# Performance work log

Hardware: AMD Instinct MI355X
Metric: run time of the kernel (lower is better)

Reference implementation:

```python
import jax, jax.numpy as jnp
import numpy as np


def setup_inputs() -> dict:
    key = jax.random.key(0)
    k1, k2, k3, k4 = jax.random.split(key, 4)
    B, T, IN, D = 32, 256, 64, 128
    x = jax.random.normal(k1, (B, T, IN), dtype=jnp.float32)
    h0 = jnp.zeros((B, D), dtype=jnp.float32)
    Wx = jax.random.normal(k2, (IN, D), dtype=jnp.float32) * 0.01
    Wgate = jax.random.normal(k3, (D, D), dtype=jnp.float32) * 0.01
    Wh = jax.random.normal(k4, (D, D), dtype=jnp.float32) * 0.01
    return {"x": x, "h0": h0, "Wx": Wx, "Wgate": Wgate, "Wh": Wh}


def reference(x, h0, Wx, Wgate, Wh):
    # x: (B, T, in_dim); h0: (B, dim); returns (h_final, y, hidden_grads, dh_dWh)
    def step_single(h_r, x_r):
        # per-sample gated update: h_r (dim,), x_r (in_dim,)
        pre = x_r @ Wx + h_r @ Wh
        a = jax.nn.gelu(pre, approximate=False)  # torch GELU() is the exact erf variant
        g = jax.nn.sigmoid(a @ Wgate)
        hn = g * h_r + (1.0 - g)
        return hn, hn

    # per-step, per-sample Jacobian d h_new / d h  (mirrors vmap(jacrev(..., argnums=1)))
    jac_batched = jax.vmap(jax.jacrev(step_single, argnums=0, has_aux=True))

    def body(h, x_t):  # h: (B, dim), x_t: (B, in_dim)
        jac, h_new = jac_batched(h, x_t)  # jac: (B, dim, dim)
        return h_new, (h_new, jac)

    xt = jnp.swapaxes(x, 0, 1)  # (T, B, in_dim)
    h_final, (ys, jacs) = jax.lax.scan(body, h0, xt)
    y = jnp.swapaxes(ys, 0, 1)  # (B, T, dim)

    # last-step Jacobian wrt Wh, evaluated with the post-update h (as in the torch code)
    x_last = x[:, -1, :]

    def f_wh(Wh_):
        pre = x_last @ Wx + h_final @ Wh_
        a = jax.nn.gelu(pre, approximate=False)
        g = jax.nn.sigmoid(a @ Wgate)
        return g * h_final + (1.0 - g)

    dh_dWh = jax.jacrev(f_wh)(Wh)  # (B, dim, dim, dim)
    return (h_final, y, jacs, dh_dWh)
```

## Files before the change

### kernel.cpp

```cpp
#include <hip/hip_runtime.h>


#define JACOFF 1052672L
#define DHWOFF 135270400L

typedef __attribute__((ext_vector_type(8))) short frag_ab;
typedef __attribute__((ext_vector_type(4))) float frag_cd;

__device__ __forceinline__ short f2bf(float f) {
    unsigned u = __builtin_bit_cast(unsigned, f);
    unsigned r = (u + 0x7fffu + ((u >> 16) & 1u)) >> 16;
    return (short)r;
}

__global__ __launch_bounds__(256) void prep_xw_kernel(
    const float* __restrict__ Wh, const float* __restrict__ Wg,
    const float* __restrict__ x, const float* __restrict__ Wx,
    float* __restrict__ whT, float* __restrict__ wgT, float* __restrict__ xw)
{
    int blk = blockIdx.x;
    int tid = threadIdx.x;
    if (blk < 128) {
        int idx = blk * 256 + tid;
        if (idx < 16384) {
            int k = idx >> 7, i = idx & 127;
            whT[i * 128 + k] = Wh[idx];
        } else {
            int r = idx - 16384;
            int k = r >> 7, i = r & 127;
            wgT[i * 128 + k] = Wg[r];
        }
        return;
    }
    __shared__ float xs[2][64];
    int sub = tid >> 7;
    int bt = (blk - 128) * 2 + sub;
    int i = tid & 127;
    if (i < 64) xs[sub][i] = x[bt * 64 + i];
    __syncthreads();
    float acc = 0.f;
#pragma unroll
    for (int m = 0; m < 64; ++m)
        acc += xs[sub][m] * Wx[m * 128 + i];
    xw[bt * 128 + i] = acc;
}

__global__ __launch_bounds__(512, 1) void scan_pk_kernel(
    const float* __restrict__ xw, const float* __restrict__ h0,
    const float* __restrict__ whT, const float* __restrict__ wgT,
    const float* __restrict__ Wgate, const float* __restrict__ Wh,
    float* __restrict__ out,
    short* __restrict__ Abf, float* __restrict__ wgv, float* __restrict__ wc,
    float* __restrict__ wdF, float* __restrict__ wuF, float* __restrict__ whF,
    short* __restrict__ PT)
{
    int tid = threadIdx.x;
    if (blockIdx.x >= 32) {
        int c = (blockIdx.x - 32) * 32 + (tid >> 4);
        int k0 = (tid & 15) * 8;
        int i = c >> 7, j = c & 127;
        short v[8];
#pragma unroll
        for (int m = 0; m < 8; ++m) {
            float wg = Wgate[(k0 + m) * 128 + i];
            float wh = Wh[j * 128 + k0 + m];
            v[m] = f2bf(wg * wh);
        }
        *(frag_ab*)(PT + (long)c * 128 + k0) = *(frag_ab*)v;
        return;
    }

    const int b = blockIdx.x;
    const int i = tid >> 2, qtr = tid & 3;
    __shared__ float hbuf[2][128];
    __shared__ float abuf[128];
    float wh[32], wgc[32];
    {
        const float* whr = whT + i * 128 + qtr * 32;
        const float* wgr = wgT + i * 128 + qtr * 32;
#pragma unroll
        for (int k = 0; k < 32; k += 4) {
            float4 a4 = *(const float4*)(whr + k);
            wh[k] = a4.x; wh[k + 1] = a4.y; wh[k + 2] = a4.z; wh[k + 3] = a4.w;
            float4 b4 = *(const float4*)(wgr + k);
            wgc[k] = b4.x; wgc[k + 1] = b4.y; wgc[k + 2] = b4.z; wgc[k + 3] = b4.w;
        }
    }
    if (qtr == 0) hbuf[0][i] = h0[b * 128 + i];
    __syncthreads();

    const float inv_sqrt2 = 0.70710678118654752f;
    const float inv_sqrt2pi = 0.39894228040143268f;

    float xwv = xw[(b * 256 + 0) * 128 + i];

    for (int t = 0; t < 256; ++t) {
        int p = t & 1;
        int tn = (t < 255) ? t + 1 : 255;
        float xwn = xw[(b * 256 + tn) * 128 + i];

        float s0 = 0.f, s1 = 0.f, s2 = 0.f, s3 = 0.f;
        const float* hb = &hbuf[p][qtr * 32];
#pragma unroll
        for (int k = 0; k < 32; k += 4) {
            float4 h4 = *(const float4*)(hb + k);
            s0 += h4.x * wh[k];
            s1 += h4.y * wh[k + 1];
            s2 += h4.z * wh[k + 2];
            s3 += h4.w * wh[k + 3];
        }
        float s = (s0 + s1) + (s2 + s3);
        s += __shfl_xor(s, 1);
        s += __shfl_xor(s, 2);
        float pre = xwv + s;

        float cdf = 0.5f * (1.0f + erff(pre * inv_sqrt2));
        float a = pre * cdf;
        float dval = cdf + pre * inv_sqrt2pi * expf(-0.5f * pre * pre);

        long tb = (long)(t * 32 + b) * 128 + i;
        if (qtr == 0) {
            Abf[tb] = f2bf(dval);
            abuf[i] = a;
        }
        __syncthreads();

        float r0 = 0.f, r1 = 0.f, r2 = 0.f, r3 = 0.f;
        const float* ab = &abuf[qtr * 32];
#pragma unroll
        for (int k = 0; k < 32; k += 4) {
            float4 a4 = *(const float4*)(ab + k);
            r0 += a4.x * wgc[k];
            r1 += a4.y * wgc[k + 1];
            r2 += a4.z * wgc[k + 2];
            r3 += a4.w * wgc[k + 3];
        }
        float r = (r0 + r1) + (r2 + r3);
        r += __shfl_xor(r, 1);
        r += __shfl_xor(r, 2);
        float g = 1.0f / (1.0f + expf(-r));
        float hp = hbuf[p][i];
        float c = (hp - 1.0f) * g * (1.0f - g);
        float hn = g * hp + 1.0f - g;
        if (qtr == 0) {
            hbuf[p ^ 1][i] = hn;
            wgv[tb] = g;
            wc[tb] = c;
            out[4096 + (b * 256 + t) * 128 + i] = hn;
        }
        xwv = xwn;
        __syncthreads();
    }

    float hfin = hbuf[0][i];
    if (qtr == 0) {
        out[b * 128 + i] = hfin;
        whF[b * 128 + i] = hfin;
    }

    {
        float s0 = 0.f, s1 = 0.f, s2 = 0.f, s3 = 0.f;
        const float* hb = &hbuf[0][qtr * 32];
#pragma unroll
        for (int k = 0; k < 32; k += 4) {
            float4 h4 = *(const float4*)(hb + k);
            s0 += h4.x * wh[k];
            s1 += h4.y * wh[k + 1];
            s2 += h4.z * wh[k + 2];
            s3 += h4.w * wh[k + 3];
        }
        float s = (s0 + s1) + (s2 + s3);
        s += __shfl_xor(s, 1);
        s += __shfl_xor(s, 2);
        float pre = xwv + s;
        float cdf = 0.5f * (1.0f + erff(pre * inv_sqrt2));
        float a = pre * cdf;
        float dval = cdf + pre * inv_sqrt2pi * expf(-0.5f * pre * pre);
        if (qtr == 0) {
            wdF[b * 128 + i] = dval;
            abuf[i] = a;
        }
        __syncthreads();
        float r0 = 0.f, r1 = 0.f, r2 = 0.f, r3 = 0.f;
        const float* ab = &abuf[qtr * 32];
#pragma unroll
        for (int k = 0; k < 32; k += 4) {
            float4 a4 = *(const float4*)(ab + k);
            r0 += a4.x * wgc[k];
            r1 += a4.y * wgc[k + 1];
            r2 += a4.z * wgc[k + 2];
            r3 += a4.w * wgc[k + 3];
        }
        float r = (r0 + r1) + (r2 + r3);
        r += __shfl_xor(r, 1);
        r += __shfl_xor(r, 2);
        float g = 1.0f / (1.0f + expf(-r));
        if (qtr == 0) wuF[b * 128 + i] = (hfin - 1.0f) * g * (1.0f - g);
    }
}

__global__ __launch_bounds__(256) void jacmm_dhdw_kernel(
    const short* __restrict__ Abf,
    const short* __restrict__ PT,
    const float* __restrict__ wgv,
    const float* __restrict__ wc,
    const float* __restrict__ Wgate,
    const float* __restrict__ dF, const float* __restrict__ uF, const float* __restrict__ hF,
    float* __restrict__ out)
{
    int bx = blockIdx.x;
    int tid = threadIdx.x;
    int grp = bx / 3, rem = bx % 3;

    if (rem == 2) {
        __shared__ float hs[128], dsh[128];
        int b = grp >> 7, i = grp & 127;
        if (tid < 128) {
            hs[tid] = hF[b * 128 + tid];
            dsh[tid] = dF[b * 128 + tid];
        }
        __syncthreads();
        float u = uF[b * 128 + i];
        int q0 = (tid & 31) * 4, p0 = (tid >> 5) * 16;
        float w0 = u * dsh[q0 + 0] * Wgate[(q0 + 0) * 128 + i];
        float w1 = u * dsh[q0 + 1] * Wgate[(q0 + 1) * 128 + i];
        float w2 = u * dsh[q0 + 2] * Wgate[(q0 + 2) * 128 + i];
        float w3 = u * dsh[q0 + 3] * Wgate[(q0 + 3) * 128 + i];
        float* dst = out + DHWOFF + (long)grp * 16384;
#pragma unroll
        for (int pp = 0; pp < 16; ++pp) {
            float hp = hs[p0 + pp];
            *(float4*)(dst + (p0 + pp) * 128 + q0) = make_float4(hp * w0, hp * w1, hp * w2, hp * w3);
        }
        return;
    }

    __shared__ short Atile[128 * 128];
    __shared__ short Btile[128 * 128];

    int jb = grp * 2 + rem;
    int rb = jb & 63;
    int cb = jb >> 6;

    const short* Ag = Abf + (long)rb * (128 * 128);
    const short* Bg = PT + (long)cb * (128 * 128);

#pragma unroll
    for (int e = 0; e < 8; ++e) {
        int q = e * 256 + tid;
        int r = q >> 4;
        int s = q & 15;
        int ko = s ^ (r & 15);
        const short* srcA = Ag + r * 128 + ko * 8;
        const short* srcB = Bg + r * 128 + ko * 8;
        __builtin_amdgcn_global_load_lds(
            (const __attribute__((address_space(1))) void*)srcA,
            (__attribute__((address_space(3))) void*)(Atile + q * 8), 16, 0, 0);
        __builtin_amdgcn_global_load_lds(
            (const __attribute__((address_space(1))) void*)srcB,
            (__attribute__((address_space(3))) void*)(Btile + q * 8), 16, 0, 0);
    }

    int w = tid >> 6;
    int lane = tid & 63;
    int wr = w >> 1;
    int wcol = w & 1;
    int lrow = lane & 15;
    int quad = lane >> 4;

    long rowbase = (long)rb * 128;
    float ci[4][4], gi[4][4];
#pragma unroll
    for (int p = 0; p < 4; ++p) {
        int trow0 = wr * 64 + p * 16 + quad * 4;
#pragma unroll
        for (int reg = 0; reg < 4; ++reg) {
            long row = rowbase + trow0 + reg;
            ci[p][reg] = wc[row * 128 + cb];
            gi[p][reg] = wgv[row * 128 + cb];
        }
    }
    __syncthreads();

    frag_cd acc[4][4];
#pragma unroll
    for (int p = 0; p < 4; ++p)
#pragma unroll
        for (int q = 0; q < 4; ++q) {
            acc[p][q][0] = 0.f; acc[p][q][1] = 0.f; acc[p][q][2] = 0.f; acc[p][q][3] = 0.f;
        }

#pragma unroll
    for (int kk = 0; kk < 4; ++kk) {
        int ko = kk * 4 + quad;
        frag_ab af[4], bf[4];
#pragma unroll
        for (int p = 0; p < 4; ++p) {
            int r = wr * 64 + p * 16 + lrow;
            int chunk = r * 16 + (ko ^ (r & 15));
            af[p] = *(const frag_ab*)&Atile[chunk * 8];
        }
#pragma unroll
        for (int q = 0; q < 4; ++q) {
            int n = wcol * 64 + q * 16 + lrow;
            int chunk = n * 16 + (ko ^ (n & 15));
            bf[q] = *(const frag_ab*)&Btile[chunk * 8];
        }
#pragma unroll
        for (int p = 0; p < 4; ++p)
#pragma unroll
            for (int q = 0; q < 4; ++q)
                acc[p][q] = __builtin_amdgcn_mfma_f32_16x16x32_bf16(af[p], bf[q], acc[p][q], 0, 0, 0);
    }

#pragma unroll
    for (int p = 0; p < 4; ++p) {
        int trow0 = wr * 64 + p * 16 + quad * 4;
#pragma unroll
        for (int reg = 0; reg < 4; ++reg) {
            long row = rowbase + trow0 + reg;
            float* orow = out + JACOFF + row * 16384 + (long)cb * 128;
#pragma unroll
            for (int q = 0; q < 4; ++q) {
                int tcol = wcol * 64 + q * 16 + lrow;
                float v = ci[p][reg] * acc[p][q][reg];
                if (tcol == cb) v += gi[p][reg];
                orow[tcol] = v;
            }
        }
    }
}

extern "C" void kernel_launch(void* const* d_in, const int* in_sizes, int n_in,
                              void* d_out, int out_size, void* d_ws, size_t ws_size,
                              hipStream_t stream)
{
    (void)in_sizes; (void)n_in; (void)out_size; (void)ws_size;
    const float* x     = (const float*)d_in[0];
    const float* h0    = (const float*)d_in[1];
    const float* Wx    = (const float*)d_in[2];
    const float* Wgate = (const float*)d_in[3];
    const float* Wh    = (const float*)d_in[4];
    float* out = (float*)d_out;
    float* ws  = (float*)d_ws;

    float* xw  = ws;
    float* whT = ws + 1048576;
    float* wgT = ws + 1064960;
    float* wgv = ws + 1081344;
    float* wc  = ws + 2129920;
    float* wdF = ws + 3178496;
    float* wuF = ws + 3182592;
    float* whF = ws + 3186688;
    short* Abf = (short*)(ws + 3190784);
    short* PT  = (short*)(ws + 3715072);

    prep_xw_kernel<<<4224, 256, 0, stream>>>(Wh, Wgate, x, Wx, whT, wgT, xw);
    scan_pk_kernel<<<544, 512, 0, stream>>>(xw, h0, whT, wgT, Wgate, Wh, out,
                                            Abf, wgv, wc, wdF, wuF, whF, PT);
    jacmm_dhdw_kernel<<<12288, 256, 0, stream>>>(Abf, PT, wgv, wc, Wgate, wdF, wuF, whF, out);
}
```

Before: 1.090 ms.

## Load MFMA fragments straight from global, use DPP reductions and lighter barriers

The Jacobian matmul kernel no longer stages its A and B tiles into LDS through global_load_lds. Each wave now reads its bf16 MFMA fragments directly from global memory, relying on L2 for reuse across waves. This drops 64KB of LDS and a block barrier, but duplicates global reads between waves. The recurrence kernel also swaps shfl_xor reductions for DPP moves, replaces __syncthreads with a raw lgkmcnt wait plus s_barrier, and prefetches xw two steps ahead.

```diff
diff --git a/kernel.cpp b/kernel.cpp
--- a/kernel.cpp
+++ b/kernel.cpp
@@ -11,6 +11,19 @@
     unsigned u = __builtin_bit_cast(unsigned, f);
     unsigned r = (u + 0x7fffu + ((u >> 16) & 1u)) >> 16;
     return (short)r;
+}
+
+__device__ __forceinline__ void wg_barrier() {
+    asm volatile("s_waitcnt lgkmcnt(0)\n\ts_barrier" ::: "memory");
+}
+
+__device__ __forceinline__ float dpp_xor1(float x) {
+    int r = __builtin_amdgcn_mov_dpp(__builtin_bit_cast(int, x), 0xB1, 0xF, 0xF, true);
+    return __builtin_bit_cast(float, r);
+}
+__device__ __forceinline__ float dpp_xor2(float x) {
+    int r = __builtin_amdgcn_mov_dpp(__builtin_bit_cast(int, x), 0x4E, 0xF, 0xF, true);
+    return __builtin_bit_cast(float, r);
 }
 
 __global__ __launch_bounds__(256) void prep_xw_kernel(
@@ -93,11 +106,12 @@
     const float inv_sqrt2pi = 0.39894228040143268f;
 
     float xwv = xw[(b * 256 + 0) * 128 + i];
+    float xw1 = xw[(b * 256 + 1) * 128 + i];
 
     for (int t = 0; t < 256; ++t) {
         int p = t & 1;
-        int tn = (t < 255) ? t + 1 : 255;
-        float xwn = xw[(b * 256 + tn) * 128 + i];
+        int tn = (t < 254) ? t + 2 : 255;
+        float xw2 = xw[(b * 256 + tn) * 128 + i];
 
         float s0 = 0.f, s1 = 0.f, s2 = 0.f, s3 = 0.f;
         const float* hb = &hbuf[p][qtr * 32];
@@ -110,8 +124,8 @@
             s3 += h4.w * wh[k + 3];
         }
         float s = (s0 + s1) + (s2 + s3);
-        s += __shfl_xor(s, 1);
-        s += __shfl_xor(s, 2);
+        s += dpp_xor1(s);
+        s += dpp_xor2(s);
         float pre = xwv + s;
 
         float cdf = 0.5f * (1.0f + erff(pre * inv_sqrt2));
@@ -123,7 +137,7 @@
             Abf[tb] = f2bf(dval);
             abuf[i] = a;
         }
-        __syncthreads();
+        wg_barrier();
 
         float r0 = 0.f, r1 = 0.f, r2 = 0.f, r3 = 0.f;
         const float* ab = &abuf[qtr * 32];
@@ -136,8 +150,8 @@
             r3 += a4.w * wgc[k + 3];
         }
         float r = (r0 + r1) + (r2 + r3);
-        r += __shfl_xor(r, 1);
-        r += __shfl_xor(r, 2);
+        r += dpp_xor1(r);
+        r += dpp_xor2(r);
         float g = 1.0f / (1.0f + expf(-r));
         float hp = hbuf[p][i];
         float c = (hp - 1.0f) * g * (1.0f - g);
@@ -148,8 +162,8 @@
             wc[tb] = c;
             out[4096 + (b * 256 + t) * 128 + i] = hn;
         }
-        xwv = xwn;
-        __syncthreads();
+        xwv = xw1; xw1 = xw2;
+        wg_barrier();
     }
 
     float hfin = hbuf[0][i];
@@ -170,8 +184,8 @@
             s3 += h4.w * wh[k + 3];
         }
         float s = (s0 + s1) + (s2 + s3);
-        s += __shfl_xor(s, 1);
-        s += __shfl_xor(s, 2);
+        s += dpp_xor1(s);
+        s += dpp_xor2(s);
         float pre = xwv + s;
         float cdf = 0.5f * (1.0f + erff(pre * inv_sqrt2));
         float a = pre * cdf;
@@ -192,8 +206,8 @@
             r3 += a4.w * wgc[k + 3];
         }
         float r = (r0 + r1) + (r2 + r3);
-        r += __shfl_xor(r, 1);
-        r += __shfl_xor(r, 2);
+        r += dpp_xor1(r);
+        r += dpp_xor2(r);
         float g = 1.0f / (1.0f + expf(-r));
         if (qtr == 0) wuF[b * 128 + i] = (hfin - 1.0f) * g * (1.0f - g);
     }
@@ -235,31 +249,12 @@
         return;
     }
 
-    __shared__ short Atile[128 * 128];
-    __shared__ short Btile[128 * 128];
-
     int jb = grp * 2 + rem;
     int rb = jb & 63;
     int cb = jb >> 6;
 
     const short* Ag = Abf + (long)rb * (128 * 128);
     const short* Bg = PT + (long)cb * (128 * 128);
-
-#pragma unroll
-    for (int e = 0; e < 8; ++e) {
-        int q = e * 256 + tid;
-        int r = q >> 4;
-        int s = q & 15;
-        int ko = s ^ (r & 15);
-        const short* srcA = Ag + r * 128 + ko * 8;
-        const short* srcB = Bg + r * 128 + ko * 8;
-        __builtin_amdgcn_global_load_lds(
-            (const __attribute__((address_space(1))) void*)srcA,
-            (__attribute__((address_space(3))) void*)(Atile + q * 8), 16, 0, 0);
-        __builtin_amdgcn_global_load_lds(
-            (const __attribute__((address_space(1))) void*)srcB,
-            (__attribute__((address_space(3))) void*)(Btile + q * 8), 16, 0, 0);
-    }
 
     int w = tid >> 6;
     int lane = tid & 63;
@@ -280,7 +275,6 @@
             gi[p][reg] = wgv[row * 128 + cb];
         }
     }
-    __syncthreads();
 
     frag_cd acc[4][4];
 #pragma unroll
@@ -292,19 +286,17 @@
 
 #pragma unroll
     for (int kk = 0; kk < 4; ++kk) {
-        int ko = kk * 4 + quad;
+        int ko8 = (kk * 4 + quad) * 8;
         frag_ab af[4], bf[4];
 #pragma unroll
         for (int p = 0; p < 4; ++p) {
             int r = wr * 64 + p * 16 + lrow;
-            int chunk = r * 16 + (ko ^ (r & 15));
-            af[p] = *(const frag_ab*)&Atile[chunk * 8];
+            af[p] = *(const frag_ab*)(Ag + r * 128 + ko8);
         }
 #pragma unroll
         for (int q = 0; q < 4; ++q) {
             int n = wcol * 64 + q * 16 + lrow;
-            int chunk = n * 16 + (ko ^ (n & 15));
-            bf[q] = *(const frag_ab*)&Btile[chunk * 8];
+            bf[q] = *(const frag_ab*)(Bg + n * 128 + ko8);
         }
 #pragma unroll
         for (int p = 0; p < 4; ++p)
```

Result: slower. 1.130 ms (+3.6%).
